# Performance work log

Measured on AMD Instinct MI355X. Metric: run time of the kernel, lower is better.

The kernel has to match this reference:

```python
import jax, jax.numpy as jnp
import numpy as np

NUM_ITERATIONS = 3
EPS = 1e-12


def _squash(s):
    # s: (..., V). squash(s) = |s|^2 * s / ((1+|s|^2) * |s|)
    sq = jnp.sum(s * s, axis=-1, keepdims=True)
    return sq * s / ((1.0 + sq) * jnp.sqrt(sq))


def setup_inputs() -> dict:
    key = jax.random.key(0)
    kx, kw = jax.random.split(key)
    B, L, P, V, Q = 16, 64, 1024, 64, 16
    x = jax.random.normal(kx, (B, P, Q), dtype=jnp.float32)
    W = 0.01 * jax.random.normal(kw, (L, P, V, Q), dtype=jnp.float32)
    return {"x": x, "W": W}


def reference(x, W):
    # u_hat[b,l,p,v] = sum_q W[l,p,v,q] * x[b,p,q]
    u_hat = jnp.einsum('lpvq,bpq->blpv', W, x)  # (B, L, P, V)
    B, L, P, V = u_hat.shape
    b_ij = jnp.zeros((B, L, P), dtype=u_hat.dtype)
    c_ij = None
    v = None
    for it in range(NUM_ITERATIONS):  # small fixed unroll
        c_ij = jax.nn.softmax(b_ij, axis=1)  # softmax over latent caps
        s = jnp.einsum('blp,blpv->blv', c_ij, u_hat)
        v = _squash(s)  # (B, L, V)
        if it < NUM_ITERATIONS - 1:
            # agreement update: b_ij += <v_j, u_hat>
            b_ij = b_ij + jnp.einsum('blv,blpv->blp', v, u_hat)
    # T-score: coupling entropy over latent axis, per primary capsule
    cT = jnp.swapaxes(c_ij, 1, 2)  # (B, P, L)
    entropy = -jnp.sum(cT * jnp.log(cT + EPS), axis=-1)  # (B, P)
    T = jnp.mean(1.0 - entropy / np.log(float(L)))
    # D-score: max over caps of population std (over batch) of activation norms
    v_norm = jnp.linalg.norm(v, axis=-1)  # (B, L)
    D = jnp.max(jnp.std(v_norm, axis=0))
    return v, T, D
```

## Files before the change

kernel.cpp:

```cpp
#include <hip/hip_runtime.h>
#include <hip/hip_bf16.h>

#define B 16
#define L 64
#define P 1024
#define V 64
#define Q 16
#define LN64 4.158883083359672f

#define CHBC 16
#define NCH_BC (P / CHBC)

typedef unsigned short ushort8_t __attribute__((ext_vector_type(8)));

typedef const __attribute__((address_space(1))) void* gld_gptr_t;
typedef __attribute__((address_space(3))) void* gld_lptr_t;

static __device__ __forceinline__ float bf2f(ushort u) {
    return __uint_as_float(((unsigned int)u) << 16);
}
static __device__ __forceinline__ ushort f2bf(float f) {
    unsigned int x = __float_as_uint(f);
    unsigned int r = (x + 0x7fffu + ((x >> 16) & 1u)) >> 16;
    return (ushort)r;
}

static __device__ __forceinline__ float wsum64(float v) {
#pragma unroll
    for (int m = 32; m > 0; m >>= 1) v += __shfl_xor(v, m, 64);
    return v;
}
static __device__ __forceinline__ float wmax64(float v) {
#pragma unroll
    for (int m = 32; m > 0; m >>= 1) v = fmaxf(v, __shfl_xor(v, m, 64));
    return v;
}

__global__ __launch_bounds__(256) void k_uhat(const float* __restrict__ Wt,
                                              const float* __restrict__ x,
                                              ushort* __restrict__ uhat) {
    const int t = threadIdx.x;
    const int w = t >> 6;
    const int lane = t & 63;
    const int p = blockIdx.x >> 1;
    const int l0 = (blockIdx.x & 1) * 32;
    const int b   = (t >> 3) & 15;
    const int vo  = t & 7;
    const int lih = t >> 7;
    const int vosw = vo & 3;

    __shared__ float xs[B * Q];
    __shared__ char wls[6][4096];

    {
        const int bb = t >> 4, q = t & 15;
        xs[t] = x[((size_t)bb * P + p) * Q + q];
    }
    __syncthreads();

    float xr[16];
    {
        const float4* xb = reinterpret_cast<const float4*>(&xs[b * Q]);
#pragma unroll
        for (int q4 = 0; q4 < 4; ++q4) {
            float4 v4 = xb[q4];
            xr[q4 * 4 + 0] = v4.x; xr[q4 * 4 + 1] = v4.y;
            xr[q4 * 4 + 2] = v4.z; xr[q4 * 4 + 3] = v4.w;
        }
    }

    const int sc = w * 64 + lane;
    const int nsrc = (sc & ~3) | ((sc & 3) ^ ((sc >> 5) & 3));
    const char* gW = (const char*)Wt + ((size_t)l0 * P + p) * (V * Q * 4)
                     + (size_t)nsrc * 16;
    const size_t LSTRIDE = (size_t)P * V * Q * 4;

    ushort* ub = uhat + ((size_t)(b * L + l0) * P + p) * V + vo * 8;

#define STAGE(li_)                                                            \
    __builtin_amdgcn_global_load_lds(                                         \
        (gld_gptr_t)(gW + (size_t)(li_) * LSTRIDE),                           \
        (gld_lptr_t)(&wls[(li_) % 6][w * 1024]), 16, 0, 0);

#define COMPUTE(s)                                                            \
    {                                                                         \
        const char* sb = &wls[(2 * (s)) % 6][0] + lih * 4096;                 \
        float d[8];                                                           \
        _Pragma("unroll")                                                     \
        for (int j = 0; j < 8; ++j) {                                         \
            const char* rb = sb + (vo * 8 + j) * 64;                          \
            const float4 W0 = *(const float4*)(rb + ((0 ^ vosw) << 4));       \
            const float4 W1 = *(const float4*)(rb + ((1 ^ vosw) << 4));       \
            const float4 W2 = *(const float4*)(rb + ((2 ^ vosw) << 4));       \
            const float4 W3 = *(const float4*)(rb + ((3 ^ vosw) << 4));       \
            float u = 0.f;                                                    \
            u = fmaf(W0.x, xr[0],  u); u = fmaf(W0.y, xr[1],  u);             \
            u = fmaf(W0.z, xr[2],  u); u = fmaf(W0.w, xr[3],  u);             \
            u = fmaf(W1.x, xr[4],  u); u = fmaf(W1.y, xr[5],  u);             \
            u = fmaf(W1.z, xr[6],  u); u = fmaf(W1.w, xr[7],  u);             \
            u = fmaf(W2.x, xr[8],  u); u = fmaf(W2.y, xr[9],  u);             \
            u = fmaf(W2.z, xr[10], u); u = fmaf(W2.w, xr[11], u);             \
            u = fmaf(W3.x, xr[12], u); u = fmaf(W3.y, xr[13], u);             \
            u = fmaf(W3.z, xr[14], u); u = fmaf(W3.w, xr[15], u);             \
            d[j] = u;                                                         \
        }                                                                     \
        uint4 pk;                                                             \
        pk.x = (unsigned)f2bf(d[0]) | ((unsigned)f2bf(d[1]) << 16);           \
        pk.y = (unsigned)f2bf(d[2]) | ((unsigned)f2bf(d[3]) << 16);           \
        pk.z = (unsigned)f2bf(d[4]) | ((unsigned)f2bf(d[5]) << 16);           \
        pk.w = (unsigned)f2bf(d[6]) | ((unsigned)f2bf(d[7]) << 16);           \
        *reinterpret_cast<uint4*>(ub + (size_t)(2 * (s) + lih) * P * V) = pk; \
    }

#define WAITB(N)                                                              \
    asm volatile("s_waitcnt vmcnt(" #N ")" ::: "memory");                     \
    __builtin_amdgcn_sched_barrier(0);                                        \
    __builtin_amdgcn_s_barrier();                                             \
    __builtin_amdgcn_sched_barrier(0);

    STAGE(0); STAGE(1); STAGE(2); STAGE(3);

    WAITB(2); STAGE(4); STAGE(5); COMPUTE(0);
    WAITB(3); STAGE(6); STAGE(7); COMPUTE(1);
#pragma unroll
    for (int s = 2; s <= 13; ++s) {
        WAITB(4); STAGE(2 * s + 4); STAGE(2 * s + 5); COMPUTE(s);
    }
    WAITB(4); COMPUTE(14);
    WAITB(2); COMPUTE(15);

#undef STAGE
#undef COMPUTE
#undef WAITB
}

__global__ __launch_bounds__(256) void k_s(const ushort* __restrict__ uhat,
                                           float* __restrict__ vout) {
    const int l = blockIdx.x, b = blockIdx.y;
    const int t = threadIdx.x;
    const int w = t >> 6, lane = t & 63;
    const int pl = t >> 4;
    const int vg = t & 15;

    __shared__ float4 sl[4][16];

    const ushort* up = uhat + ((size_t)(b * L + l)) * P * V + (size_t)pl * V + vg * 4;

    float4 acc = {0.f, 0.f, 0.f, 0.f};
#pragma unroll 8
    for (int i = 0; i < 64; ++i) {
        ushort4 u = *reinterpret_cast<const ushort4*>(up + (size_t)i * 16 * V);
        acc.x += bf2f(u.x); acc.y += bf2f(u.y);
        acc.z += bf2f(u.z); acc.w += bf2f(u.w);
    }
    acc.x *= (1.f / 64.f); acc.y *= (1.f / 64.f);
    acc.z *= (1.f / 64.f); acc.w *= (1.f / 64.f);
#pragma unroll
    for (int m = 16; m <= 32; m <<= 1) {
        acc.x += __shfl_xor(acc.x, m, 64);
        acc.y += __shfl_xor(acc.y, m, 64);
        acc.z += __shfl_xor(acc.z, m, 64);
        acc.w += __shfl_xor(acc.w, m, 64);
    }
    if (lane < 16) sl[w][vg] = acc;
    __syncthreads();
    if (w == 0 && lane < 16) {
        float4 s0 = sl[0][vg], s1 = sl[1][vg], s2 = sl[2][vg], s3 = sl[3][vg];
        float4 s;
        s.x = s0.x + s1.x + s2.x + s3.x;
        s.y = s0.y + s1.y + s2.y + s3.y;
        s.z = s0.z + s1.z + s2.z + s3.z;
        s.w = s0.w + s1.w + s2.w + s3.w;
        float sq = s.x * s.x + s.y * s.y + s.z * s.z + s.w * s.w;
        sq += __shfl_xor(sq, 1, 64);
        sq += __shfl_xor(sq, 2, 64);
        sq += __shfl_xor(sq, 4, 64);
        sq += __shfl_xor(sq, 8, 64);
        float f = sqrtf(sq) / (1.0f + sq);
        float4 o = {s.x * f, s.y * f, s.z * f, s.w * f};
        *reinterpret_cast<float4*>(vout + (size_t)(b * L + l) * V + vg * 4) = o;
    }
}

__global__ __launch_bounds__(512, 4) void k_bc(const ushort* __restrict__ uhat,
                                               const float* __restrict__ vv,
                                               float* __restrict__ bbuf,
                                               float* __restrict__ sp,
                                               float* __restrict__ Tsum,
                                               int add_prev, int do_T) {
    const int ch = blockIdx.x, b = blockIdx.y;
    const int p0 = ch * CHBC;
    const int t = threadIdx.x;
    const int w = t >> 6, lane = t & 63;
    const int pl8 = lane >> 3;
    const int vg8 = lane & 7;
    const int l0 = w * 8;

    __shared__ float vsh[L][V];
    __shared__ float bl[CHBC][L + 1];
    __shared__ float twv[8];

    {
        const float4* vvp = reinterpret_cast<const float4*>(vv + (size_t)b * L * V);
        float4* vshp = reinterpret_cast<float4*>(&vsh[0][0]);
#pragma unroll
        for (int i = 0; i < 2; ++i) vshp[t + i * 512] = vvp[t + i * 512];
    }

    ushort8_t ur[8][2];
    {
        const ushort* ubase = uhat + (((size_t)(b * L + l0)) * P + p0 + pl8) * V + vg8 * 8;
#pragma unroll
        for (int li = 0; li < 8; ++li) {
#pragma unroll
            for (int ph = 0; ph < 2; ++ph)
                ur[li][ph] = *reinterpret_cast<const ushort8_t*>(
                    ubase + ((size_t)li * P + ph * 8) * V);
        }
    }
    __syncthreads();

#pragma unroll
    for (int li = 0; li < 8; ++li) {
        const int l = l0 + li;
        const float4 va = *reinterpret_cast<const float4*>(&vsh[l][vg8 * 8]);
        const float4 vb = *reinterpret_cast<const float4*>(&vsh[l][vg8 * 8 + 4]);
#pragma unroll
        for (int ph = 0; ph < 2; ++ph) {
            float d;
            d = bf2f(ur[li][ph][0]) * va.x;
            d = fmaf(bf2f(ur[li][ph][1]), va.y, d);
            d = fmaf(bf2f(ur[li][ph][2]), va.z, d);
            d = fmaf(bf2f(ur[li][ph][3]), va.w, d);
            d = fmaf(bf2f(ur[li][ph][4]), vb.x, d);
            d = fmaf(bf2f(ur[li][ph][5]), vb.y, d);
            d = fmaf(bf2f(ur[li][ph][6]), vb.z, d);
            d = fmaf(bf2f(ur[li][ph][7]), vb.w, d);
            d += __shfl_xor(d, 1, 64);
            d += __shfl_xor(d, 2, 64);
            d += __shfl_xor(d, 4, 64);
            if (vg8 == 0) bl[ph * 8 + pl8][l] = d;
        }
    }
    __syncthreads();

    float tloc = 0.f;
#pragma unroll
    for (int pi = 0; pi < 2; ++pi) {
        const int pli = w * 2 + pi;
        const int p = p0 + pli;
        float bv = bl[pli][lane];
        float* bp = bbuf + ((size_t)b * P + p) * L;
        if (add_prev) bv += bp[lane];
        bp[lane] = bv;
        float m = wmax64(bv);
        float e = __expf(bv - m);
        float ssum = wsum64(e);
        float cc = e / ssum;
        bl[pli][lane] = cc;
        if (do_T) tloc += cc * __logf(64.0f * (cc + 1e-12f));
    }
    if (do_T) {
        float dsum = wsum64(tloc);
        if (lane == 0) twv[w] = dsum;
    }
    __syncthreads();
    if (do_T && t == 0) {
        float s8 = twv[0] + twv[1] + twv[2] + twv[3] +
                   twv[4] + twv[5] + twv[6] + twv[7];
        atomicAdd(Tsum, s8 * (1.0f / LN64));
    }

    float* spb = sp + (size_t)(b * NCH_BC + ch) * L * V;
#pragma unroll
    for (int li = 0; li < 8; ++li) {
        const int l = l0 + li;
        const float cA = bl[pl8][l];
        const float cB = bl[8 + pl8][l];
        float4 pa, pb;
        pa.x = cA * bf2f(ur[li][0][0]) + cB * bf2f(ur[li][1][0]);
        pa.y = cA * bf2f(ur[li][0][1]) + cB * bf2f(ur[li][1][1]);
        pa.z = cA * bf2f(ur[li][0][2]) + cB * bf2f(ur[li][1][2]);
        pa.w = cA * bf2f(ur[li][0][3]) + cB * bf2f(ur[li][1][3]);
        pb.x = cA * bf2f(ur[li][0][4]) + cB * bf2f(ur[li][1][4]);
        pb.y = cA * bf2f(ur[li][0][5]) + cB * bf2f(ur[li][1][5]);
        pb.z = cA * bf2f(ur[li][0][6]) + cB * bf2f(ur[li][1][6]);
        pb.w = cA * bf2f(ur[li][0][7]) + cB * bf2f(ur[li][1][7]);
#pragma unroll
        for (int m = 8; m <= 32; m <<= 1) {
            pa.x += __shfl_xor(pa.x, m, 64);
            pa.y += __shfl_xor(pa.y, m, 64);
            pa.z += __shfl_xor(pa.z, m, 64);
            pa.w += __shfl_xor(pa.w, m, 64);
            pb.x += __shfl_xor(pb.x, m, 64);
            pb.y += __shfl_xor(pb.y, m, 64);
            pb.z += __shfl_xor(pb.z, m, 64);
            pb.w += __shfl_xor(pb.w, m, 64);
        }
        if (pl8 == 0) {
            *reinterpret_cast<float4*>(spb + (size_t)l * V + vg8 * 8) = pa;
            *reinterpret_cast<float4*>(spb + (size_t)l * V + vg8 * 8 + 4) = pb;
        }
    }
}

__global__ __launch_bounds__(256) void k_v(const float* __restrict__ sp,
                                           float* __restrict__ vout,
                                           float* __restrict__ norms) {
    const int b = blockIdx.y;
    const int w = threadIdx.x >> 6, lane = threadIdx.x & 63;
    const int l = blockIdx.x * 4 + w;
    const float* p = sp + ((size_t)b * NCH_BC * L + l) * V + lane;
    float s = 0.f;
#pragma unroll 8
    for (int ch = 0; ch < NCH_BC; ++ch) s += p[(size_t)ch * L * V];
    float sq = wsum64(s * s);
    float f = sqrtf(sq) / (1.0f + sq);
    vout[((size_t)b * L + l) * V + lane] = s * f;
    if (norms && lane == 0) norms[b * L + l] = sq / (1.0f + sq);
}

__global__ void k_final(const float* __restrict__ Tsum,
                        const float* __restrict__ norms,
                        float* __restrict__ out) {
    const int lane = threadIdx.x & 63;
    float n[B];
    float sum = 0.f;
#pragma unroll
    for (int b = 0; b < B; ++b) { n[b] = norms[b * L + lane]; sum += n[b]; }
    const float mean = sum * (1.0f / B);
    float var = 0.f;
#pragma unroll
    for (int b = 0; b < B; ++b) { float d = n[b] - mean; var = fmaf(d, d, var); }
    var *= (1.0f / B);
    float sd = sqrtf(var);
    float D = wmax64(sd);
    if (lane == 0) {
        out[B * L * V] = Tsum[0] * (1.0f / (B * P));
        out[B * L * V + 1] = D;
    }
}

extern "C" void kernel_launch(void* const* d_in, const int* in_sizes, int n_in,
                              void* d_out, int out_size, void* d_ws, size_t ws_size,
                              hipStream_t stream) {
    const float* x = (const float*)d_in[0];
    const float* W = (const float*)d_in[1];
    float* out = (float*)d_out;

    char* ws = (char*)d_ws;
    ushort* uhat = (ushort*)ws;
    size_t off = (size_t)B * L * P * V * 2;
    float* spbuf = (float*)(ws + off); off += (size_t)B * NCH_BC * L * V * 4;
    float* vbuf  = (float*)(ws + off); off += (size_t)B * L * V * 4;
    float* bbuf  = (float*)(ws + off); off += (size_t)B * P * L * 4;
    float* norms = (float*)(ws + off); off += (size_t)B * L * 4;
    float* Tsum  = (float*)(ws + off); off += 256;

    hipMemsetAsync(Tsum, 0, sizeof(float), stream);

    hipLaunchKernelGGL(k_uhat, dim3(2048), dim3(256), 0, stream, W, x, uhat);
    hipLaunchKernelGGL(k_s, dim3(L, B), dim3(256), 0, stream, uhat, vbuf);
    hipLaunchKernelGGL(k_bc, dim3(NCH_BC, B), dim3(512), 0, stream,
                       uhat, vbuf, bbuf, spbuf, Tsum, 0, 0);
    hipLaunchKernelGGL(k_v, dim3(L / 4, B), dim3(256), 0, stream,
                       spbuf, vbuf, (float*)nullptr);
    hipLaunchKernelGGL(k_bc, dim3(NCH_BC, B), dim3(512), 0, stream,
                       uhat, vbuf, bbuf, spbuf, Tsum, 1, 1);
    hipLaunchKernelGGL(k_v, dim3(L / 4, B), dim3(256), 0, stream,
                       spbuf, out, norms);
    hipLaunchKernelGGL(k_final, dim3(1), dim3(64), 0, stream, Tsum, norms, out);
}
```

Baseline: 230.1 us.

## Restructure u_hat kernel around a per-l, 64-p tile and change u_hat layout

The u_hat kernel now has each block handle one latent capsule and 64 primary capsules, streaming W tiles through a 5-deep LDS ring with a 4-ahead prefetch. The x slice for those 64 p is staged in shared memory as packed bf16 pairs. The u_hat workspace layout changes from (B,L,P,V) to (L,B,P,V), and the consumer kernels' indexing is updated to match. The aim is longer contiguous W streaming per block and fewer blocks, at the cost of rounding x to bf16, which adds error, and fewer total blocks (1024).

```diff
diff --git a/kernel.cpp b/kernel.cpp
--- a/kernel.cpp
+++ b/kernel.cpp
@@ -24,6 +24,12 @@
     unsigned int r = (x + 0x7fffu + ((x >> 16) & 1u)) >> 16;
     return (ushort)r;
 }
+static __device__ __forceinline__ float pklo(unsigned int w) {
+    return __uint_as_float(w << 16);
+}
+static __device__ __forceinline__ float pkhi(unsigned int w) {
+    return __uint_as_float(w & 0xffff0000u);
+}
 
 static __device__ __forceinline__ float wsum64(float v) {
 #pragma unroll
@@ -42,74 +48,64 @@
     const int t = threadIdx.x;
     const int w = t >> 6;
     const int lane = t & 63;
-    const int p = blockIdx.x >> 1;
-    const int l0 = (blockIdx.x & 1) * 32;
-    const int b   = (t >> 3) & 15;
-    const int vo  = t & 7;
-    const int lih = t >> 7;
-    const int vosw = vo & 3;
-
-    __shared__ float xs[B * Q];
-    __shared__ char wls[6][4096];
-
-    {
-        const int bb = t >> 4, q = t & 15;
-        xs[t] = x[((size_t)bb * P + p) * Q + q];
-    }
-    __syncthreads();
-
-    float xr[16];
-    {
-        const float4* xb = reinterpret_cast<const float4*>(&xs[b * Q]);
-#pragma unroll
-        for (int q4 = 0; q4 < 4; ++q4) {
-            float4 v4 = xb[q4];
-            xr[q4 * 4 + 0] = v4.x; xr[q4 * 4 + 1] = v4.y;
-            xr[q4 * 4 + 2] = v4.z; xr[q4 * 4 + 3] = v4.w;
-        }
-    }
-
-    const int sc = w * 64 + lane;
-    const int nsrc = (sc & ~3) | ((sc & 3) ^ ((sc >> 5) & 3));
-    const char* gW = (const char*)Wt + ((size_t)l0 * P + p) * (V * Q * 4)
-                     + (size_t)nsrc * 16;
-    const size_t LSTRIDE = (size_t)P * V * Q * 4;
-
-    ushort* ub = uhat + ((size_t)(b * L + l0) * P + p) * V + vo * 8;
-
-#define STAGE(li_)                                                            \
+    const int l = blockIdx.x >> 4;
+    const int p0 = (blockIdx.x & 15) * 64;
+    const int b = t >> 4;
+    const int vg = t & 15;
+    const int xsw = vg & 3;
+
+    __shared__ unsigned int xls[64][B][8];
+    __shared__ char wls[5][4096];
+
+#pragma unroll
+    for (int i = 0; i < 32; ++i) {
+        const int flat = i * 256 + t;
+        const int bb = flat >> 9, rem = flat & 511;
+        const int pp = rem >> 3, j = rem & 7;
+        const float2 xv = *reinterpret_cast<const float2*>(
+            x + ((size_t)bb * P + p0 + pp) * Q + 2 * j);
+        xls[pp][bb][j] = (unsigned)f2bf(xv.x) | ((unsigned)f2bf(xv.y) << 16);
+    }
+
+    const int s = w * 64 + lane;
+    const int src = (s & ~3) | ((s & 3) ^ ((s >> 4) & 3));
+    const char* gW = (const char*)(Wt + ((size_t)l * P + p0) * (V * Q))
+                     + (size_t)src * 16;
+
+    ushort* ub = uhat + (((size_t)(l * B + b)) * P + p0) * V + vg * 4;
+
+#define STAGE(pi)                                                             \
     __builtin_amdgcn_global_load_lds(                                         \
-        (gld_gptr_t)(gW + (size_t)(li_) * LSTRIDE),                           \
-        (gld_lptr_t)(&wls[(li_) % 6][w * 1024]), 16, 0, 0);
-
-#define COMPUTE(s)                                                            \
+        (gld_gptr_t)(gW + (size_t)(pi) * 4096),                               \
+        (gld_lptr_t)(&wls[(pi) % 5][w * 1024]), 16, 0, 0);
+
+#define COMPUTE(pi)                                                           \
     {                                                                         \
-        const char* sb = &wls[(2 * (s)) % 6][0] + lih * 4096;                 \
-        float d[8];                                                           \
+        const unsigned int* xw = &xls[pi][b][0];                              \
+        const char* sb = &wls[(pi) % 5][0];                                   \
+        float d[4];                                                           \
         _Pragma("unroll")                                                     \
-        for (int j = 0; j < 8; ++j) {                                         \
-            const char* rb = sb + (vo * 8 + j) * 64;                          \
-            const float4 W0 = *(const float4*)(rb + ((0 ^ vosw) << 4));       \
-            const float4 W1 = *(const float4*)(rb + ((1 ^ vosw) << 4));       \
-            const float4 W2 = *(const float4*)(rb + ((2 ^ vosw) << 4));       \
-            const float4 W3 = *(const float4*)(rb + ((3 ^ vosw) << 4));       \
+        for (int j = 0; j < 4; ++j) {                                         \
+            const char* rb = sb + (vg * 4 + j) * 64;                          \
+            const float4 W0 = *(const float4*)(rb + ((0 ^ xsw) << 4));        \
+            const float4 W1 = *(const float4*)(rb + ((1 ^ xsw) << 4));        \
+            const float4 W2 = *(const float4*)(rb + ((2 ^ xsw) << 4));        \
+            const float4 W3 = *(const float4*)(rb + ((3 ^ xsw) << 4));        \
             float u = 0.f;                                                    \
-            u = fmaf(W0.x, xr[0],  u); u = fmaf(W0.y, xr[1],  u);             \
-            u = fmaf(W0.z, xr[2],  u); u = fmaf(W0.w, xr[3],  u);             \
-            u = fmaf(W1.x, xr[4],  u); u = fmaf(W1.y, xr[5],  u);             \
-            u = fmaf(W1.z, xr[6],  u); u = fmaf(W1.w, xr[7],  u);             \
-            u = fmaf(W2.x, xr[8],  u); u = fmaf(W2.y, xr[9],  u);             \
-            u = fmaf(W2.z, xr[10], u); u = fmaf(W2.w, xr[11], u);             \
-            u = fmaf(W3.x, xr[12], u); u = fmaf(W3.y, xr[13], u);             \
-            u = fmaf(W3.z, xr[14], u); u = fmaf(W3.w, xr[15], u);             \
+            u = fmaf(W0.x, pklo(xw[0]), u); u = fmaf(W0.y, pkhi(xw[0]), u);   \
+            u = fmaf(W0.z, pklo(xw[1]), u); u = fmaf(W0.w, pkhi(xw[1]), u);   \
+            u = fmaf(W1.x, pklo(xw[2]), u); u = fmaf(W1.y, pkhi(xw[2]), u);   \
+            u = fmaf(W1.z, pklo(xw[3]), u); u = fmaf(W1.w, pkhi(xw[3]), u);   \
+            u = fmaf(W2.x, pklo(xw[4]), u); u = fmaf(W2.y, pkhi(xw[4]), u);   \
+            u = fmaf(W2.z, pklo(xw[5]), u); u = fmaf(W2.w, pkhi(xw[5]), u);   \
+            u = fmaf(W3.x, pklo(xw[6]), u); u = fmaf(W3.y, pkhi(xw[6]), u);   \
+            u = fmaf(W3.z, pklo(xw[7]), u); u = fmaf(W3.w, pkhi(xw[7]), u);   \
             d[j] = u;                                                         \
         }                                                                     \
-        uint4 pk;                                                             \
+        uint2 pk;                                                             \
         pk.x = (unsigned)f2bf(d[0]) | ((unsigned)f2bf(d[1]) << 16);           \
         pk.y = (unsigned)f2bf(d[2]) | ((unsigned)f2bf(d[3]) << 16);           \
-        pk.z = (unsigned)f2bf(d[4]) | ((unsigned)f2bf(d[5]) << 16);           \
-        pk.w = (unsigned)f2bf(d[6]) | ((unsigned)f2bf(d[7]) << 16);           \
-        *reinterpret_cast<uint4*>(ub + (size_t)(2 * (s) + lih) * P * V) = pk; \
+        *reinterpret_cast<uint2*>(ub + (size_t)(pi) * V) = pk;                \
     }
 
 #define WAITB(N)                                                              \
@@ -119,15 +115,22 @@
     __builtin_amdgcn_sched_barrier(0);
 
     STAGE(0); STAGE(1); STAGE(2); STAGE(3);
-
-    WAITB(2); STAGE(4); STAGE(5); COMPUTE(0);
-    WAITB(3); STAGE(6); STAGE(7); COMPUTE(1);
-#pragma unroll
-    for (int s = 2; s <= 13; ++s) {
-        WAITB(4); STAGE(2 * s + 4); STAGE(2 * s + 5); COMPUTE(s);
-    }
-    WAITB(4); COMPUTE(14);
-    WAITB(2); COMPUTE(15);
+    __syncthreads();
+
+    WAITB(3); STAGE(4); COMPUTE(0);
+    WAITB(4); STAGE(5); COMPUTE(1);
+    WAITB(5); STAGE(6); COMPUTE(2);
+    WAITB(6); STAGE(7); COMPUTE(3);
+#pragma unroll 1
+    for (int pi = 4; pi <= 59; ++pi) {
+        WAITB(7);
+        STAGE(pi + 4);
+        COMPUTE(pi);
+    }
+    WAITB(7); COMPUTE(60);
+    WAITB(6); COMPUTE(61);
+    WAITB(5); COMPUTE(62);
+    WAITB(4); COMPUTE(63);
 
 #undef STAGE
 #undef COMPUTE
@@ -144,7 +147,7 @@
 
     __shared__ float4 sl[4][16];
 
-    const ushort* up = uhat + ((size_t)(b * L + l)) * P * V + (size_t)pl * V + vg * 4;
+    const ushort* up = uhat + ((size_t)(l * B + b)) * P * V + (size_t)pl * V + vg * 4;
 
     float4 acc = {0.f, 0.f, 0.f, 0.f};
 #pragma unroll 8
@@ -209,13 +212,13 @@
 
     ushort8_t ur[8][2];
     {
-        const ushort* ubase = uhat + (((size_t)(b * L + l0)) * P + p0 + pl8) * V + vg8 * 8;
+        const ushort* ubase = uhat + (((size_t)(l0 * B + b)) * P + p0 + pl8) * V + vg8 * 8;
 #pragma unroll
         for (int li = 0; li < 8; ++li) {
 #pragma unroll
             for (int ph = 0; ph < 2; ++ph)
                 ur[li][ph] = *reinterpret_cast<const ushort8_t*>(
-                    ubase + ((size_t)li * P + ph * 8) * V);
+                    ubase + (size_t)li * B * P * V + (size_t)ph * 8 * V);
         }
     }
     __syncthreads();
@@ -359,7 +362,7 @@
 
     hipMemsetAsync(Tsum, 0, sizeof(float), stream);
 
-    hipLaunchKernelGGL(k_uhat, dim3(2048), dim3(256), 0, stream, W, x, uhat);
+    hipLaunchKernelGGL(k_uhat, dim3(1024), dim3(256), 0, stream, W, x, uhat);
     hipLaunchKernelGGL(k_s, dim3(L, B), dim3(256), 0, stream, uhat, vbuf);
     hipLaunchKernelGGL(k_bc, dim3(NCH_BC, B), dim3(512), 0, stream,
                        uhat, vbuf, bbuf, spbuf, Tsum, 0, 0);
```

New measurement: 309.6 us. 34.5% more time.
